# Kernel tuning notes

Hardware: AMD Instinct MI355X
Metric: run time of the kernel (lower is better)

Reference implementation:

```python
import jax, jax.numpy as jnp
import numpy as np

B, L, H, NH = 4, 2048, 1024, 8
DK = H // NH   # head_k_dim = 128
DV = H // NH   # head_v_dim = 128
CONV_K, FIR_S, FIR_L = 4, 3, 31
CMAX = 0.2
EPS = 1e-5
CHUNK = 32


def _l2norm(x):
    return x * jax.lax.rsqrt(jnp.sum(x * x, -1, keepdims=True) + 1e-6)


def _rms(x, w):
    return x * jax.lax.rsqrt(jnp.mean(x * x, -1, keepdims=True) + EPS) * w


def _causal_conv(x, w):
    # x: [b, l, d], w: [d, K] depthwise causal FIR (ShortConvolution)
    K = w.shape[1]
    l = x.shape[1]
    xp = jnp.pad(x, ((0, 0), (K - 1, 0), (0, 0)))
    return sum(xp[:, i:i + l, :] * w[:, i][None, None, :] for i in range(K))


def _fir(x, w):
    # x: [b, l, h, d], w: [h, d, K] per-head depthwise causal FIR
    K = w.shape[-1]
    l = x.shape[1]
    xp = jnp.pad(x, ((0, 0), (K - 1, 0), (0, 0), (0, 0)))
    return sum(xp[:, i:i + l] * w[:, :, i][None, None] for i in range(K))


def _delta_rule_chunkwise(q, k, v, beta, chunk=CHUNK):
    # q,k: [b,h,L,dk]; v: [b,h,L,dv]; beta: [b,h,L]; L % chunk == 0
    b, h, Ln, dk = q.shape
    dv = v.shape[-1]
    n = Ln // chunk
    q = _l2norm(q)
    k = _l2norm(k)
    v = v * beta[..., None]
    kb = k * beta[..., None]
    rs = lambda t: t.reshape(b, h, n, chunk, t.shape[-1])
    qc, kc, vc, kbc = rs(q), rs(k), rs(v), rs(kb)
    mask_incl = jnp.triu(jnp.ones((chunk, chunk), dtype=bool), 0)
    mask_strict = jnp.triu(jnp.ones((chunk, chunk), dtype=bool), 1)
    # UT / WY transform: sequential Gaussian-elimination over chunk rows
    attn = jnp.where(mask_incl, 0.0, -(kbc @ jnp.swapaxes(kc, -1, -2)))
    for i in range(1, chunk):
        row = attn[..., i, :]                                   # [b,h,n,c]
        upd = jnp.einsum('bhnj,bhnjk->bhnk', row, attn[..., :i])  # [b,h,n,i]
        attn = attn.at[..., i, :i].add(upd)
    attn = attn + jnp.eye(chunk, dtype=attn.dtype)
    u = attn @ vc    # [b,h,n,c,dv]
    w = attn @ kbc   # [b,h,n,c,dk]
    # sequential scan over chunks carrying state S [b,h,dk,dv]
    mv = lambda t: jnp.moveaxis(t, 2, 0)  # [n,b,h,c,d]
    def step(S, xs):
        q_i, k_i, u_i, w_i = xs
        attn_local = jnp.where(mask_strict, 0.0, q_i @ jnp.swapaxes(k_i, -1, -2))
        u_new = u_i - w_i @ S
        o_i = q_i @ S + attn_local @ u_new
        S = S + jnp.swapaxes(k_i, -1, -2) @ u_new
        return S, o_i
    S0 = jnp.zeros((b, h, dk, dv), dtype=q.dtype)
    S, o = jax.lax.scan(step, S0, (mv(qc), mv(kc), mv(u), mv(w)))
    o = jnp.moveaxis(o, 0, 2).reshape(b, h, Ln, dv)
    return o, S


def _forward(hidden_states, Wq, Wk, Wv, Wb, conv_q_w, conv_k_w, conv_v_w,
             fir_short_w, fir_long_w, floor_W, floor_b, fus_W1, fus_b1,
             fus_W2, fus_b2, norm_pf_w, norm_o_w, Wo):
    b, l, _ = hidden_states.shape
    hs = hidden_states
    q_lin = jax.nn.silu(_causal_conv(hs @ Wq, conv_q_w))
    k_lin = jax.nn.silu(_causal_conv(hs @ Wk, conv_k_w))
    v_lin = jax.nn.silu(_causal_conv(hs @ Wv, conv_v_w))
    q = q_lin.reshape(b, l, NH, DK)
    k = k_lin.reshape(b, l, NH, DK)
    v_direct = v_lin.reshape(b, l, NH, DV)
    beta = jax.nn.sigmoid(hs @ Wb)  # [b,l,h]
    delta_out_t, _ = _delta_rule_chunkwise(
        jnp.transpose(q, (0, 2, 1, 3)), jnp.transpose(k, (0, 2, 1, 3)),
        jnp.transpose(v_direct, (0, 2, 1, 3)), jnp.transpose(beta, (0, 2, 1)))
    delta_out = jnp.transpose(delta_out_t, (0, 2, 1, 3))  # [b,l,h,dv]
    local_short = _fir(v_direct, fir_short_w)
    local_long = _fir(v_direct, fir_long_w)
    floor = jax.nn.sigmoid(hs @ floor_W + floor_b) * CMAX  # [b,l,h]
    fus = jax.nn.gelu(hs @ fus_W1 + fus_b1, approximate=False) @ fus_W2 + fus_b2
    fus = fus.reshape(b, l, NH, 4)
    p_value = jax.nn.sigmoid(fus[..., 3]) * (1.0 - floor)  # context share >= floor
    ctx = jax.nn.softmax(fus[..., :3], axis=-1) * (1.0 - p_value)[..., None]
    o = (ctx[..., 0, None] * local_short + ctx[..., 1, None] * local_long
         + ctx[..., 2, None] * delta_out + p_value[..., None] * v_direct)
    o = _rms(o, norm_pf_w)
    o = _rms(o, norm_o_w)
    return o.reshape(b, l, NH * DV) @ Wo


def setup_inputs() -> dict:
    key = jax.random.key(0)
    ks = jax.random.split(key, 16)
    n = lambda k, shape, s=0.02: jax.random.normal(k, shape, jnp.float32) * s
    fus_b2 = jnp.zeros((NH * 4,), jnp.float32).at[3::4].set(4.0)
    return {
        'hidden_states': jax.random.normal(ks[0], (B, L, H), jnp.float32),
        'Wq': n(ks[1], (H, H)), 'Wk': n(ks[2], (H, H)), 'Wv': n(ks[3], (H, H)),
        'Wb': n(ks[4], (H, NH)),
        'conv_q_w': n(ks[5], (H, CONV_K), 0.2),
        'conv_k_w': n(ks[6], (H, CONV_K), 0.2),
        'conv_v_w': n(ks[7], (H, CONV_K), 0.2),
        'fir_short_w': n(ks[8], (NH, DV, FIR_S), 0.2),
        'fir_long_w': n(ks[9], (NH, DV, FIR_L), 0.2),
        'floor_W': n(ks[10], (H, NH)),
        'floor_b': jnp.full((NH,), float(np.log(CMAX / (1 - CMAX))), jnp.float32),
        'fus_W1': n(ks[11], (H, 2 * H)), 'fus_b1': jnp.zeros((2 * H,), jnp.float32),
        'fus_W2': n(ks[12], (2 * H, NH * 4)), 'fus_b2': fus_b2,
        'norm_pf_w': jnp.ones((DV,), jnp.float32),
        'norm_o_w': jnp.ones((DV,), jnp.float32),
        'Wo': n(ks[13], (H, H)),
    }


def reference(hidden_states, Wq, Wk, Wv, Wb, conv_q_w, conv_k_w, conv_v_w,
              fir_short_w, fir_long_w, floor_W, floor_b, fus_W1, fus_b1,
              fus_W2, fus_b2, norm_pf_w, norm_o_w, Wo):
    return _forward(hidden_states, Wq, Wk, Wv, Wb, conv_q_w, conv_k_w, conv_v_w,
                    fir_short_w, fir_long_w, floor_W, floor_b, fus_W1, fus_b1,
                    fus_W2, fus_b2, norm_pf_w, norm_o_w, Wo)
```

## Files before the change

kernel.cpp:

```cpp
#include <hip/hip_runtime.h>
#include <hip/hip_bf16.h>
#include <cstdint>
#include <cstddef>

#define DEVI static __device__ __forceinline__

typedef __attribute__((ext_vector_type(4))) float f32x4;
typedef __attribute__((ext_vector_type(8))) short s16x8;
typedef unsigned short u16;
typedef unsigned int u32;

DEVI float bf2f(u16 u){ u32 x = ((u32)u) << 16; float f; __builtin_memcpy(&f, &x, 4); return f; }
DEVI u16 f2bf(float f){ u32 x; __builtin_memcpy(&x, &f, 4); u32 r = x + 0x7fffu + ((x >> 16) & 1u); return (u16)(r >> 16); }
DEVI float sigm(float x){ return 1.0f / (1.0f + __expf(-x)); }
DEVI f32x4 mfma16(s16x8 a, s16x8 b, f32x4 c){ return __builtin_amdgcn_mfma_f32_16x16x32_bf16(a, b, c, 0, 0, 0); }
DEVI s16x8 pack8(float4 a, float4 b){
  s16x8 v;
  v[0]=(short)f2bf(a.x); v[1]=(short)f2bf(a.y); v[2]=(short)f2bf(a.z); v[3]=(short)f2bf(a.w);
  v[4]=(short)f2bf(b.x); v[5]=(short)f2bf(b.y); v[6]=(short)f2bf(b.z); v[7]=(short)f2bf(b.w);
  return v;
}
DEVI u32 pkbf(float lo, float hi){
  u32 d; asm("v_cvt_pk_bf16_f32 %0, %1, %2" : "=v"(d) : "v"(lo), "v"(hi));
  return d;
}
DEVI s16x8 ld_tr(const u16* p){
  short4 a = *(const short4*)p;
  short4 b = *(const short4*)(p + 4);
  s16x8 v; v[0]=a.x; v[1]=a.y; v[2]=a.z; v[3]=a.w; v[4]=b.x; v[5]=b.y; v[6]=b.z; v[7]=b.w;
  return v;
}

#define GLL16(gp, lp) __builtin_amdgcn_global_load_lds( \
    (const __attribute__((address_space(1))) void*)(gp), \
    (__attribute__((address_space(3))) void*)(lp), 16, 0, 0)

__global__ __launch_bounds__(256) void cvt_bf16_k(const float* __restrict__ src, u16* __restrict__ dst, int n4){
  int i = blockIdx.x * 256 + threadIdx.x;
  if (i < n4){
    float4 v = ((const float4*)src)[i];
    ushort4 o; o.x = f2bf(v.x); o.y = f2bf(v.y); o.z = f2bf(v.z); o.w = f2bf(v.w);
    ((ushort4*)dst)[i] = o;
  }
}

DEVI void transpose_tile(const float* src, u16* dst, int K, int N,
                         int n0, int k0, int t){
  __shared__ float tile[32][33];
  const int cc = t & 31, rb = t >> 5;
  #pragma unroll
  for (int it = 0; it < 4; ++it){ int rr = rb + it*8; tile[rr][cc] = src[(size_t)(k0+rr)*N + n0 + cc]; }
  __syncthreads();
  #pragma unroll
  for (int it = 0; it < 4; ++it){ int rr = rb + it*8; dst[(size_t)(n0+rr)*K + k0 + cc] = f2bf(tile[cc][rr]); }
}

__global__ __launch_bounds__(256) void prep_k(
    const float* __restrict__ Wq, const float* __restrict__ Wk, const float* __restrict__ Wv,
    const float* __restrict__ W1, const float* __restrict__ Wo,
    const float* __restrict__ W2, const float* __restrict__ Wb, const float* __restrict__ Wfl,
    u16* __restrict__ wqT, u16* __restrict__ wkT, u16* __restrict__ wvT,
    u16* __restrict__ w1T, u16* __restrict__ woT,
    u16* __restrict__ w2p, u16* __restrict__ wbp)
{
  const int blk = blockIdx.x, t = threadIdx.x;
  if (blk < 3072){
    const int which = blk >> 10, tile = blk & 1023;
    const float* src = (which == 0) ? Wq : (which == 1) ? Wk : Wv;
    u16* dst = (which == 0) ? wqT : (which == 1) ? wkT : wvT;
    transpose_tile(src, dst, 1024, 1024, (tile & 31)*32, (tile >> 5)*32, t);
  } else if (blk < 5120){
    const int tile = blk - 3072;
    transpose_tile(W1, w1T, 1024, 2048, (tile & 63)*32, (tile >> 6)*32, t);
  } else if (blk < 6144){
    const int tile = blk - 5120;
    transpose_tile(Wo, woT, 1024, 1024, (tile & 31)*32, (tile >> 5)*32, t);
  } else if (blk < 6272){
    if (t < 64){
      const int i = blk - 6144, kt = i & 63, nt = i >> 6;
      const int lane = t, g = lane >> 4, r = lane & 15;
      float v[8];
      #pragma unroll
      for (int j=0;j<8;++j) v[j] = W2[(size_t)(kt*32 + g*8 + j)*32 + nt*16 + r];
      *(s16x8*)(w2p + (((size_t)kt*2 + nt)*64 + lane)*8) =
          pack8(make_float4(v[0],v[1],v[2],v[3]), make_float4(v[4],v[5],v[6],v[7]));
    }
  } else {
    if (t < 64){
      const int kt = blk - 6272;
      const int lane = t, g = lane >> 4, r = lane & 15;
      float v[8];
      #pragma unroll
      for (int j=0;j<8;++j){
        const int k = kt*32 + g*8 + j;
        v[j] = (r < 8) ? Wb[(size_t)k*8 + r] : Wfl[(size_t)k*8 + (r-8)];
      }
      *(s16x8*)(wbp + ((size_t)kt*64 + lane)*8) =
          pack8(make_float4(v[0],v[1],v[2],v[3]), make_float4(v[4],v[5],v[6],v[7]));
    }
  }
}

template<int EPI>
__global__ __launch_bounds__(256, 2) void gemm_bt(
    const u16* __restrict__ A, const u16* __restrict__ Bt, void* __restrict__ Cout,
    const float* __restrict__ bias, int M, int N, int K)
{
  __shared__ __align__(16) u16 As[128*64];
  __shared__ __align__(16) u16 Bs[128*64];
  const int t = threadIdx.x;
  const int lane = t & 63, w = t >> 6;
  const int wr = w >> 1, wc = w & 1;
  const int g = lane >> 4, r16 = lane & 15;
  const int nwg = gridDim.x * gridDim.y;
  const int bid = blockIdx.x + blockIdx.y * gridDim.x;
  const int swz = (bid & 7) * (nwg >> 3) + (bid >> 3);
  const int m0 = (swz / gridDim.x) * 128, n0 = (swz % gridDim.x) * 128;
  f32x4 acc[4][4];
  #pragma unroll
  for (int i=0;i<4;++i){ f32x4 z = {0,0,0,0}; acc[i][0]=z; acc[i][1]=z; acc[i][2]=z; acc[i][3]=z; }
  const int NK = K / 64;
  const int slot_l = w*64 + lane;
  for (int kt = 0; kt < NK; ++kt){
    __syncthreads();
    #pragma unroll
    for (int j=0;j<4;++j){
      const int sl = j*256 + slot_l;
      const int row = sl >> 3, ch = sl & 7;
      const int chs = ch ^ (row & 7);
      GLL16(A  + (size_t)(m0+row)*K + kt*64 + chs*8, As + (size_t)(j*256 + w*64)*8);
      GLL16(Bt + (size_t)(n0+row)*K + kt*64 + chs*8, Bs + (size_t)(j*256 + w*64)*8);
    }
    __syncthreads();
    #pragma unroll
    for (int kh = 0; kh < 2; ++kh){
      s16x8 af[4], bf_[4];
      #pragma unroll
      for (int i=0;i<4;++i){
        const int arow = wr*64 + i*16 + r16;
        af[i]  = *(const s16x8*)(As + (size_t)arow*64 + (((4*kh+g) ^ (arow&7)))*8);
        const int brow = wc*64 + i*16 + r16;
        bf_[i] = *(const s16x8*)(Bs + (size_t)brow*64 + (((4*kh+g) ^ (brow&7)))*8);
      }
      #pragma unroll
      for (int mi=0;mi<4;++mi)
        #pragma unroll
        for (int ni=0;ni<4;++ni)
          acc[mi][ni] = mfma16(af[mi], bf_[ni], acc[mi][ni]);
    }
  }
  #pragma unroll
  for (int mi=0;mi<4;++mi)
    #pragma unroll
    for (int ni=0;ni<4;++ni){
      const int col = n0 + wc*64 + ni*16 + r16;
      #pragma unroll
      for (int i=0;i<4;++i){
        const int row = m0 + wr*64 + mi*16 + g*4 + i;
        float v = acc[mi][ni][i];
        if (EPI == 0){
          ((u16*)Cout)[(size_t)row*N + col] = f2bf(v);
        } else if (EPI == 1){
          float x = v + bias[col];
          x = 0.5f * x * (1.0f + erff(x * 0.70710678118f));
          ((u16*)Cout)[(size_t)row*N + col] = f2bf(x);
        } else if (EPI == 2){
          ((float*)Cout)[(size_t)row*N + col] = v;
        } else {
          ((u16*)Cout)[(size_t)(col >> 10)*8388608 + (size_t)row*1024 + (col & 1023)] = f2bf(v);
        }
      }
    }
}

__global__ __launch_bounds__(64) void beta_floor_k(
    const u16* __restrict__ hsb, const u16* __restrict__ wbp, const float* __restrict__ flb,
    float* __restrict__ beta, float* __restrict__ flo)
{
  const int m0 = blockIdx.x * 16;
  const int lane = threadIdx.x, g = lane >> 4, r = lane & 15;
  f32x4 acc0 = {0,0,0,0}, acc1 = {0,0,0,0};
  #pragma unroll 4
  for (int kt = 0; kt < 32; kt += 2){
    s16x8 a0 = *(const s16x8*)(hsb + (size_t)(m0+r)*1024 + kt*32 + g*8);
    s16x8 b0 = *(const s16x8*)(wbp + ((size_t)kt*64 + lane)*8);
    s16x8 a1 = *(const s16x8*)(hsb + (size_t)(m0+r)*1024 + (kt+1)*32 + g*8);
    s16x8 b1 = *(const s16x8*)(wbp + ((size_t)(kt+1)*64 + lane)*8);
    acc0 = mfma16(a0, b0, acc0);
    acc1 = mfma16(a1, b1, acc1);
  }
  const float fb = (r >= 8) ? flb[r-8] : 0.f;
  #pragma unroll
  for (int i=0;i<4;++i){
    const int row = m0 + g*4 + i;
    const float v = acc0[i] + acc1[i];
    if (r < 8) beta[(size_t)row*8 + r] = sigm(v);
    else       flo [(size_t)row*8 + (r-8)] = 0.2f * sigm(v + fb);
  }
}

__global__ __launch_bounds__(256) void conv_silu_k(
    const u16* __restrict__ qraw, const u16* __restrict__ kraw, const u16* __restrict__ vraw,
    const float* __restrict__ cwq, const float* __restrict__ cwk, const float* __restrict__ cwv,
    u16* __restrict__ vdir, u16* __restrict__ qn, u16* __restrict__ kn)
{
  const int blk = blockIdx.x;
  const int b = blk >> 7, lt = blk & 127;
  const int l0 = lt * 16;
  const int t = threadIdx.x, c0 = t * 4;
  float wq[16], wk[16], wv[16];
  #pragma unroll
  for (int cc=0; cc<4; ++cc){
    float4 a = *(const float4*)(cwq + (size_t)(c0+cc)*4);
    wq[cc*4+0]=a.x; wq[cc*4+1]=a.y; wq[cc*4+2]=a.z; wq[cc*4+3]=a.w;
    float4 bq = *(const float4*)(cwk + (size_t)(c0+cc)*4);
    wk[cc*4+0]=bq.x; wk[cc*4+1]=bq.y; wk[cc*4+2]=bq.z; wk[cc*4+3]=bq.w;
    float4 c = *(const float4*)(cwv + (size_t)(c0+cc)*4);
    wv[cc*4+0]=c.x; wv[cc*4+1]=c.y; wv[cc*4+2]=c.z; wv[cc*4+3]=c.w;
  }
  float hq[3][4], hk[3][4], hv[3][4];
  #pragma unroll
  for (int i=0;i<3;++i){
    const int ls = l0 - 3 + i;
    if (ls >= 0){
      const size_t base = ((size_t)(b << 11) + ls)*1024 + c0;
      union{ ushort4 v; u16 s[4]; } xq, xk, xv;
      xq.v = *(const ushort4*)(qraw + base);
      xk.v = *(const ushort4*)(kraw + base);
      xv.v = *(const ushort4*)(vraw + base);
      #pragma unroll
      for (int cc=0;cc<4;++cc){ hq[i][cc]=bf2f(xq.s[cc]); hk[i][cc]=bf2f(xk.s[cc]); hv[i][cc]=bf2f(xv.s[cc]); }
    } else {
      #pragma unroll
      for (int cc=0;cc<4;++cc){ hq[i][cc]=0.f; hk[i][cc]=0.f; hv[i][cc]=0.f; }
    }
  }
  float cq[4], ck4[4], cv4[4], nq[4], nk[4], nv[4];
  {
    const size_t base = ((size_t)(b << 11) + l0)*1024 + c0;
    union{ ushort4 v; u16 s[4]; } xq, xk, xv;
    xq.v = *(const ushort4*)(qraw + base);
    xk.v = *(const ushort4*)(kraw + base);
    xv.v = *(const ushort4*)(vraw + base);
    #pragma unroll
    for (int cc=0;cc<4;++cc){ cq[cc]=bf2f(xq.s[cc]); ck4[cc]=bf2f(xk.s[cc]); cv4[cc]=bf2f(xv.s[cc]); }
  }
  const int head = c0 >> 7, d0 = c0 & 127;
  for (int rr = 0; rr < 16; ++rr){
    const int l = l0 + rr;
    if (rr < 15){
      const size_t base = ((size_t)(b << 11) + l + 1)*1024 + c0;
      union{ ushort4 v; u16 s[4]; } xq, xk, xv;
      xq.v = *(const ushort4*)(qraw + base);
      xk.v = *(const ushort4*)(kraw + base);
      xv.v = *(const ushort4*)(vraw + base);
      #pragma unroll
      for (int cc=0;cc<4;++cc){ nq[cc]=bf2f(xq.s[cc]); nk[cc]=bf2f(xk.s[cc]); nv[cc]=bf2f(xv.s[cc]); }
    }
    float qa[4], ka[4], va[4];
    #pragma unroll
    for (int cc=0; cc<4; ++cc){
      qa[cc] = hq[0][cc]*wq[cc*4+0] + hq[1][cc]*wq[cc*4+1] + hq[2][cc]*wq[cc*4+2] + cq[cc]*wq[cc*4+3];
      ka[cc] = hk[0][cc]*wk[cc*4+0] + hk[1][cc]*wk[cc*4+1] + hk[2][cc]*wk[cc*4+2] + ck4[cc]*wk[cc*4+3];
      va[cc] = hv[0][cc]*wv[cc*4+0] + hv[1][cc]*wv[cc*4+1] + hv[2][cc]*wv[cc*4+2] + cv4[cc]*wv[cc*4+3];
    }
    #pragma unroll
    for (int cc=0; cc<4; ++cc){
      qa[cc] = qa[cc]*sigm(qa[cc]); ka[cc] = ka[cc]*sigm(ka[cc]); va[cc] = va[cc]*sigm(va[cc]);
    }
    const int grow = (b << 11) + l;
    ushort4 ov; ov.x=f2bf(va[0]); ov.y=f2bf(va[1]); ov.z=f2bf(va[2]); ov.w=f2bf(va[3]);
    *(ushort4*)(vdir + (size_t)grow*1024 + c0) = ov;
    float ssq = 0.f, ssk = 0.f;
    #pragma unroll
    for (int cc=0; cc<4; ++cc){ ssq += qa[cc]*qa[cc]; ssk += ka[cc]*ka[cc]; }
    #pragma unroll
    for (int m=1; m<32; m<<=1){ ssq += __shfl_xor(ssq, m, 64); ssk += __shfl_xor(ssk, m, 64); }
    const float rq = rsqrtf(ssq + 1e-6f), rk = rsqrtf(ssk + 1e-6f);
    const size_t ob = (((size_t)(b*8 + head))*2048 + l)*128 + d0;
    ushort4 oq, ok;
    oq.x=f2bf(qa[0]*rq); oq.y=f2bf(qa[1]*rq); oq.z=f2bf(qa[2]*rq); oq.w=f2bf(qa[3]*rq);
    ok.x=f2bf(ka[0]*rk); ok.y=f2bf(ka[1]*rk); ok.z=f2bf(ka[2]*rk); ok.w=f2bf(ka[3]*rk);
    *(ushort4*)(qn + ob) = oq;
    *(ushort4*)(kn + ob) = ok;
    #pragma unroll
    for (int cc=0; cc<4; ++cc){
      hq[0][cc]=hq[1][cc]; hq[1][cc]=hq[2][cc]; hq[2][cc]=cq[cc];  cq[cc]=nq[cc];
      hk[0][cc]=hk[1][cc]; hk[1][cc]=hk[2][cc]; hk[2][cc]=ck4[cc]; ck4[cc]=nk[cc];
      hv[0][cc]=hv[1][cc]; hv[1][cc]=hv[2][cc]; hv[2][cc]=cv4[cc]; cv4[cc]=nv[cc];
    }
  }
}

__global__ __launch_bounds__(64) void fus2_k(
    const u16* __restrict__ A, const u16* __restrict__ w2p, const float* __restrict__ b2,
    float* __restrict__ out)
{
  const int m0 = blockIdx.x * 16;
  const int lane = threadIdx.x, g = lane >> 4, r = lane & 15;
  f32x4 acc[2][2];
  #pragma unroll
  for (int nt=0;nt<2;++nt){ f32x4 z = {0,0,0,0}; acc[nt][0]=z; acc[nt][1]=z; }
  #pragma unroll 4
  for (int kt = 0; kt < 64; ++kt){
    s16x8 af = *(const s16x8*)(A + (size_t)(m0+r)*2048 + kt*32 + g*8);
    s16x8 b0 = *(const s16x8*)(w2p + (((size_t)kt*2 + 0)*64 + lane)*8);
    s16x8 b1 = *(const s16x8*)(w2p + (((size_t)kt*2 + 1)*64 + lane)*8);
    acc[0][kt&1] = mfma16(af, b0, acc[0][kt&1]);
    acc[1][kt&1] = mfma16(af, b1, acc[1][kt&1]);
  }
  #pragma unroll
  for (int nt=0;nt<2;++nt){
    const float bb = b2[nt*16 + r];
    #pragma unroll
    for (int i=0;i<4;++i)
      out[(size_t)(m0 + g*4 + i)*32 + nt*16 + r] = acc[nt][0][i] + acc[nt][1][i] + bb;
  }
}

__global__ __launch_bounds__(256, 2) void ut_k(
    const u16* __restrict__ qn, const u16* __restrict__ kn,
    const u16* __restrict__ vdir, const float* __restrict__ beta,
    u16* __restrict__ alocp, u16* __restrict__ updk,
    u16* __restrict__ wpk, u16* __restrict__ knpk, u16* __restrict__ qpk)
{
  __shared__ __align__(16) char smem[39680];
  u16*  k_s = (u16*)smem;
  float* Tm = (float*)smem;
  float* Gm = (float*)(smem + 8192);
  float* al = (float*)(smem + 12416);
  float* wl = (float*)(smem + 8192);
  u16*  knT = (u16*)(smem + 17024);
  u16*  vbT = (u16*)(smem + 28288);
  float* bet = (float*)(smem + 39552);

  const int blk = blockIdx.x;
  const int ic = blk & 63, bh = blk >> 6;
  const int b = bh >> 3, h = bh & 7;
  const int l0 = ic * 32;
  const int t = threadIdx.x;
  const int lane = t & 63, w = t >> 6;
  const int g = lane >> 4, r = lane & 15;
  const int mt = w >> 1, nt_g = w & 1;

  const size_t gqk = ((size_t)bh*2048 + l0)*128;

  {
    const int row = t >> 3, sseg = t & 7;
    #pragma unroll
    for (int ss=0; ss<2; ++ss){
      const int s = sseg + ss*8;
      int4 kv = *(const int4*)(kn + gqk + (size_t)row*128 + s*8);
      *(int4*)((char*)k_s + row*256 + ((s ^ (row&7))*16)) = kv;
    }
  }
  {
    const int rp = t & 15, cs = t >> 4;
    const int r0 = 2*rp, r1 = 2*rp + 1;
    union { s16x8 v; u16 u[8]; } k0, k1, v0, v1;
    k0.v = *(const s16x8*)(kn + gqk + (size_t)r0*128 + cs*8);
    k1.v = *(const s16x8*)(kn + gqk + (size_t)r1*128 + cs*8);
    v0.v = *(const s16x8*)(vdir + ((size_t)b*2048 + l0 + r0)*1024 + h*128 + cs*8);
    v1.v = *(const s16x8*)(vdir + ((size_t)b*2048 + l0 + r1)*1024 + h*128 + cs*8);
    const float be0 = beta[((size_t)b*2048 + l0 + r0)*8 + h];
    const float be1 = beta[((size_t)b*2048 + l0 + r1)*8 + h];
    if (t < 32) bet[t] = beta[((size_t)b*2048 + l0 + t)*8 + h];
    #pragma unroll
    for (int i=0;i<8;++i){
      const int d = cs*8 + i;
      *(u32*)(knT + (size_t)d*44 + r0) = (u32)k0.u[i] | ((u32)k1.u[i] << 16);
      u32 lo = f2bf(bf2f(v0.u[i]) * be0);
      u32 hi = f2bf(bf2f(v1.u[i]) * be1);
      *(u32*)(vbT + (size_t)d*44 + r0) = lo | (hi << 16);
    }
  }
  __syncthreads();

  {
    f32x4 gacc = {0,0,0,0}, aacc = {0,0,0,0};
    #pragma unroll
    for (int kt=0; kt<4; ++kt){
      s16x8 afk = *(const s16x8*)(kn + gqk + (size_t)(mt*16+r)*128 + kt*32 + g*8);
      s16x8 afq = *(const s16x8*)(qn + gqk + (size_t)(mt*16+r)*128 + kt*32 + g*8);
      if (nt_g == 0)
        *(s16x8*)(qpk + ((((size_t)blk*2 + mt)*4 + kt)*64 + lane)*8) = afq;
      const int brow = nt_g*16 + r;
      s16x8 bfrag = *(const s16x8*)((const char*)k_s + brow*256 + (((kt*4+g) ^ (brow&7))*16));
      gacc = mfma16(afk, bfrag, gacc);
      aacc = mfma16(afq, bfrag, aacc);
    }
    #pragma unroll
    for (int i=0;i<4;++i){
      const int rr = mt*16 + g*4 + i, cc = nt_g*16 + r;
      Gm[rr*33 + cc] = gacc[i];
      al[rr*36 + cc] = (cc <= rr) ? aacc[i] : 0.f;
    }
  }
  __syncthreads();

  if (w == 0){
    const int kk = lane & 15, grp = (lane >> 4) & 1, b0 = grp*16;
    float tc[16];
    #pragma unroll
    for (int j=0;j<16;++j)
      tc[j] = (j > kk) ? (-bet[b0+j] * Gm[(b0+j)*33 + b0+kk]) : 0.f;
    #pragma unroll
    for (int i=1;i<16;++i){
      float upd = 0.f;
      #pragma unroll
      for (int j=0;j<i;++j) upd += __shfl(tc[i], (lane & 48) + j, 64) * tc[j];
      if (kk < i) tc[i] += upd;
    }
    if (lane < 32){
      #pragma unroll
      for (int j=0;j<16;++j) Tm[(b0+j)*36 + b0+kk] = tc[j] + ((j == kk) ? 1.f : 0.f);
      if (grp == 1){
        #pragma unroll
        for (int j=0;j<16;++j) Tm[j*36 + 16 + kk] = 0.f;
      }
    }
  } else if (w == 1){
    #pragma unroll
    for (int m2=0; m2<2; ++m2){
      float4 z0 = *(const float4*)(al + (m2*16+r)*36 + g*8);
      float4 z1 = *(const float4*)(al + (m2*16+r)*36 + g*8 + 4);
      *(s16x8*)(alocp + (((size_t)blk*2 + m2)*64 + lane)*8) = pack8(z0, z1);
    }
  } else {
    #pragma unroll
    for (int q2=0; q2<4; ++q2){
      const int mtd = (w-2)*4 + q2;
      s16x8 vv = ld_tr(knT + (size_t)(mtd*16+r)*44 + g*8);
      *(s16x8*)(knpk + (((size_t)blk*8 + mtd)*64 + lane)*8) = vv;
    }
  }
  __syncthreads();

  {
    const int kP = t >> 4, cP = t & 15;
    float p = 0.f;
    #pragma unroll
    for (int m=0;m<16;++m) p += Gm[(16+kP)*33 + m] * Tm[m*36 + cP];
    al[kP*36 + cP] = -bet[16+kP] * p;
  }
  __syncthreads();

  {
    const int rT = t >> 4, cT = t & 15;
    float s = 0.f;
    #pragma unroll
    for (int k=0;k<16;++k) s += Tm[(16+rT)*36 + 16 + k] * al[k*36 + cT];
    Tm[(16+rT)*36 + cT] = s;
  }
  __syncthreads();

  {
    float bb[8];
    #pragma unroll
    for (int i=0;i<8;++i) bb[i] = bet[g*8+i];
    s16x8 tA[2];
    #pragma unroll
    for (int m2=0; m2<2; ++m2){
      float4 x0 = *(const float4*)(Tm + (m2*16+r)*36 + g*8);
      float4 x1 = *(const float4*)(Tm + (m2*16+r)*36 + g*8 + 4);
      tA[m2] = pack8(x0, x1);
    }
    #pragma unroll
    for (int rr2=0; rr2<2; ++rr2){
      const int nt = rr2*4 + w;
      s16x8 bu   = ld_tr(vbT + (size_t)(nt*16+r)*44 + g*8);
      s16x8 braw = ld_tr(knT + (size_t)(nt*16+r)*44 + g*8);
      s16x8 bw;
      #pragma unroll
      for (int i=0;i<8;++i) bw[i] = (short)f2bf(bf2f((u16)braw[i]) * bb[i]);
      f32x4 zz = {0,0,0,0};
      f32x4 du0 = mfma16(tA[0], bu, zz);
      f32x4 du1 = mfma16(tA[1], bu, zz);
      f32x4 dw0 = mfma16(tA[0], bw, zz);
      f32x4 dw1 = mfma16(tA[1], bw, zz);
      *(s16x8*)(updk + (((size_t)blk*8 + nt)*64 + lane)*8) =
          pack8(make_float4(du0[0],du0[1],du0[2],du0[3]),
                make_float4(du1[0],du1[1],du1[2],du1[3]));
      #pragma unroll
      for (int i=0;i<4;++i){
        wl[(      g*4 + i)*68 + (nt&3)*16 + r] = -dw0[i];
        wl[(16 +  g*4 + i)*68 + (nt&3)*16 + r] = -dw1[i];
      }
      __syncthreads();
      {
        const int mtp = w >> 1, ktp = rr2*2 + (w & 1);
        float4 y0 = *(const float4*)(wl + (mtp*16+r)*68 + (ktp&1)*32 + g*8);
        float4 y1 = *(const float4*)(wl + (mtp*16+r)*68 + (ktp&1)*32 + g*8 + 4);
        *(s16x8*)(wpk + ((((size_t)blk*2 + mtp)*4 + ktp)*64 + lane)*8) = pack8(y0, y1);
      }
      __syncthreads();
    }
  }
}

struct SBuf {
  s16x8 uraw;
  s16x8 wf[8];
  s16x8 qf[8];
  s16x8 a0, a1;
  s16x8 kf[8];
};

DEVI void scan_load(SBuf& b, const u16* up, const u16* wp, const u16* qp,
                    const u16* ap, const u16* kp){
  b.uraw = *(const s16x8*)(up);
  #pragma unroll
  for (int j=0;j<8;++j) b.wf[j] = *(const s16x8*)(wp + j*512);
  #pragma unroll
  for (int j=0;j<8;++j) b.qf[j] = *(const s16x8*)(qp + j*512);
  b.a0 = *(const s16x8*)(ap);
  b.a1 = *(const s16x8*)(ap + 512);
  #pragma unroll
  for (int j=0;j<8;++j) b.kf[j] = *(const s16x8*)(kp + j*512);
}

DEVI void scan_step(const SBuf& b, f32x4* Sf, u16* dptr,
                    int srcA, int srcB, bool hi, int r, int g){
  u32 pk0[8], pk1[8];
  #pragma unroll
  for (int m=0;m<8;++m){
    pk0[m] = pkbf(Sf[m][0], Sf[m][1]);
    pk1[m] = pkbf(Sf[m][2], Sf[m][3]);
  }
  s16x8 sf[4];
  #pragma unroll
  for (int kt=0;kt<4;++kt){
    u32 eA0 = __shfl(pk0[kt*2],   srcA, 64), oA0 = __shfl(pk0[kt*2+1], srcA, 64);
    u32 eA1 = __shfl(pk1[kt*2],   srcA, 64), oA1 = __shfl(pk1[kt*2+1], srcA, 64);
    u32 eB0 = __shfl(pk0[kt*2],   srcB, 64), oB0 = __shfl(pk0[kt*2+1], srcB, 64);
    u32 eB1 = __shfl(pk1[kt*2],   srcB, 64), oB1 = __shfl(pk1[kt*2+1], srcB, 64);
    union { u32 w[4]; s16x8 v; } uw;
    uw.w[0] = hi ? oA0 : eA0;
    uw.w[1] = hi ? oA1 : eA1;
    uw.w[2] = hi ? oB0 : eB0;
    uw.w[3] = hi ? oB1 : eB1;
    sf[kt] = uw.v;
  }
  f32x4 unA, unB, unA2 = {0,0,0,0}, unB2 = {0,0,0,0};
  #pragma unroll
  for (int i=0;i<4;++i){ unA[i] = bf2f((u16)b.uraw[i]); unB[i] = bf2f((u16)b.uraw[4+i]); }
  unA  = mfma16(b.wf[0], sf[0], unA);
  unA2 = mfma16(b.wf[2], sf[2], unA2);
  unB  = mfma16(b.wf[4], sf[0], unB);
  unB2 = mfma16(b.wf[6], sf[2], unB2);
  unA  = mfma16(b.wf[1], sf[1], unA);
  unA2 = mfma16(b.wf[3], sf[3], unA2);
  unB  = mfma16(b.wf[5], sf[1], unB);
  unB2 = mfma16(b.wf[7], sf[3], unB2);
  f32x4 o0 = {0,0,0,0}, o1 = {0,0,0,0};
  #pragma unroll
  for (int kt=0;kt<4;++kt){
    o0 = mfma16(b.qf[kt],   sf[kt], o0);
    o1 = mfma16(b.qf[4+kt], sf[kt], o1);
  }
  unA = unA + unA2;
  unB = unB + unB2;
  u32 a0p0 = pkbf(unA[0], unA[1]), a0p1 = pkbf(unA[2], unA[3]);
  u32 a1p0 = pkbf(unB[0], unB[1]), a1p1 = pkbf(unB[2], unB[3]);
  u32 w00 = __shfl(a0p0, srcA, 64), w10 = __shfl(a1p0, srcA, 64);
  u32 w01 = __shfl(a0p1, srcA, 64), w11 = __shfl(a1p1, srcA, 64);
  u32 w02 = __shfl(a0p0, srcB, 64), w12 = __shfl(a1p0, srcB, 64);
  u32 w03 = __shfl(a0p1, srcB, 64), w13 = __shfl(a1p1, srcB, 64);
  union { u32 w[4]; s16x8 v; } uu;
  uu.w[0] = hi ? w10 : w00;
  uu.w[1] = hi ? w11 : w01;
  uu.w[2] = hi ? w12 : w02;
  uu.w[3] = hi ? w13 : w03;
  const s16x8 uf = uu.v;
  o0 = mfma16(b.a0, uf, o0);
  o1 = mfma16(b.a1, uf, o1);
  #pragma unroll
  for (int i=0;i<4;++i){
    dptr[(size_t)(g*4+i)*128]    = f2bf(o0[i]);
    dptr[(size_t)(16+g*4+i)*128] = f2bf(o1[i]);
  }
  #pragma unroll
  for (int m=0;m<8;++m) Sf[m] = mfma16(b.kf[m], uf, Sf[m]);
}

__global__ __launch_bounds__(64, 1) void scan_k(
    const u16* __restrict__ qpk, const u16* __restrict__ wpk,
    const u16* __restrict__ updk, const u16* __restrict__ alocp,
    const u16* __restrict__ knpk, u16* __restrict__ delta)
{
  const int blk = blockIdx.x;
  const int sl = blk >> 5, bh = blk & 31;
  const int lane = threadIdx.x;
  const int g = lane >> 4, r = lane & 15;
  const int srcA = (g & 1)*32 + r;
  const int srcB = srcA + 16;
  const bool hi = (g >= 2);
  f32x4 Sf[8];
  #pragma unroll
  for (int m=0;m<8;++m){ f32x4 z = {0,0,0,0}; Sf[m] = z; }

  const u16* upB = updk + ((size_t)bh*64*8 + sl)*512 + (size_t)lane*8;
  const u16* wpB = wpk  + (size_t)bh*64*4096 + (size_t)lane*8;
  const u16* qpB = qpk  + (size_t)bh*64*4096 + (size_t)lane*8;
  const u16* apB = alocp + (size_t)bh*64*1024 + (size_t)lane*8;
  const u16* kpB = knpk + (size_t)bh*64*4096 + (size_t)lane*8;
  u16*       dB  = delta + (size_t)bh*2048*128 + sl*16 + r;

  #define LD(buf, n) scan_load(buf, upB + (size_t)(n)*4096, wpB + (size_t)(n)*4096, \
                               qpB + (size_t)(n)*4096, apB + (size_t)(n)*1024, \
                               kpB + (size_t)(n)*4096)
  #define ST(buf, n) scan_step(buf, Sf, dB + (size_t)(n)*4096, srcA, srcB, hi, r, g)

  SBuf A, B, C;
  LD(A, 0); LD(B, 1);
  for (int ic = 0; ic < 63; ic += 3){
    LD(C, ic+2);
    ST(A, ic);
    if (ic + 3 < 64) LD(A, ic+3);
    ST(B, ic+1);
    if (ic + 4 < 64) LD(B, ic+4);
    ST(C, ic+2);
  }
  ST(A, 63);
  #undef LD
  #undef ST
}

__global__ __launch_bounds__(256) void fuse_k(
    const u16* __restrict__ vdir, const u16* __restrict__ delta,
    const float* __restrict__ fusv, const float* __restrict__ flo,
    const float* __restrict__ fsw, const float* __restrict__ flw,
    const float* __restrict__ wpf, const float* __restrict__ wno,
    u16* __restrict__ ofin)
{
  __shared__ float fl_t[31][128];
  const int blk = blockIdx.x;
  const int lt = blk & 31, h = (blk >> 5) & 7, b = blk >> 8;
  const int t = threadIdx.x;
  const int w = t >> 6, lane = t & 63;
  const int d0 = lane * 2;
  const int l0 = lt*64 + w*16;
  for (int j = t; j < 3968; j += 256){
    const int d = j / 31, i = j - d*31;
    fl_t[i][d] = flw[(size_t)h*3968 + j];
  }
  __syncthreads();
  float wlo[46], whi[46];
  #pragma unroll
  for (int j = 0; j < 46; ++j){
    const int ls = l0 - 30 + j;
    u32 x = 0;
    if (ls >= 0) x = *(const u32*)(vdir + ((size_t)b*2048 + ls)*1024 + h*128 + d0);
    wlo[j] = bf2f((u16)(x & 0xffffu));
    whi[j] = bf2f((u16)(x >> 16));
  }
  float lg0[16], lg1[16];
  #pragma unroll
  for (int rr = 0; rr < 16; ++rr){ lg0[rr] = 0.f; lg1[rr] = 0.f; }
  #pragma unroll
  for (int i = 0; i < 31; ++i){
    const float2 wv = *(const float2*)&fl_t[i][d0];
    #pragma unroll
    for (int rr = 0; rr < 16; ++rr){
      lg0[rr] += wlo[rr + i] * wv.x;
      lg1[rr] += whi[rr + i] * wv.y;
    }
  }
  const float wp0 = wpf[d0], wp1 = wpf[d0+1];
  const float wn0 = wno[d0], wn1 = wno[d0+1];
  float fs0[3], fs1[3];
  #pragma unroll
  for (int i=0;i<3;++i){
    fs0[i] = fsw[((size_t)h*128 + d0)*3 + i];
    fs1[i] = fsw[((size_t)h*128 + d0 + 1)*3 + i];
  }
  #pragma unroll
  for (int rr = 0; rr < 16; ++rr){
    const int l = l0 + rr;
    const float* fr = fusv + ((size_t)b*2048 + l)*32 + h*4;
    const float f0=fr[0], f1=fr[1], f2=fr[2], f3=fr[3];
    const float flv = flo[((size_t)b*2048 + l)*8 + h];
    const float p = sigm(f3) * (1.f - flv);
    const float mx = fmaxf(f0, fmaxf(f1, f2));
    const float e0 = __expf(f0-mx), e1 = __expf(f1-mx), e2 = __expf(f2-mx);
    const float inv = (1.f - p) / (e0 + e1 + e2);
    const float c0 = e0*inv, c1 = e1*inv, c2 = e2*inv;
    const float sh0 = wlo[rr+28]*fs0[0] + wlo[rr+29]*fs0[1] + wlo[rr+30]*fs0[2];
    const float sh1 = whi[rr+28]*fs1[0] + whi[rr+29]*fs1[1] + whi[rr+30]*fs1[2];
    const u32 dl2 = *(const u32*)(delta + (((size_t)(b*8 + h))*2048 + l)*128 + d0);
    const float dlx = bf2f((u16)(dl2 & 0xffffu)), dly = bf2f((u16)(dl2 >> 16));
    float o0 = c0*sh0 + c1*lg0[rr] + c2*dlx + p*wlo[rr+30];
    float o1 = c0*sh1 + c1*lg1[rr] + c2*dly + p*whi[rr+30];
    const float b0 = o0*wp0, b1 = o1*wp1;
    float ss = o0*o0 + o1*o1;
    float tt = b0*b0 + b1*b1;
    #pragma unroll
    for (int m=1; m<64; m<<=1){
      ss += __shfl_xor(ss, m, 64);
      tt += __shfl_xor(tt, m, 64);
    }
    const float r1 = rsqrtf(ss * (1.f/128.f) + 1e-5f);
    const float r2 = rsqrtf(r1*r1*tt * (1.f/128.f) + 1e-5f);
    const u32 h0 = f2bf(o0*r1*wp0*r2*wn0), h1 = f2bf(o1*r1*wp1*r2*wn1);
    *(u32*)(ofin + ((size_t)b*2048 + l)*1024 + h*128 + d0) = h0 | (h1 << 16);
  }
}

constexpr size_t OFF_HSB  = 0;
constexpr size_t OFF_WQT  = 16777216;
constexpr size_t OFF_WKT  = 18874368;
constexpr size_t OFF_WVT  = 20971520;
constexpr size_t OFF_W1T  = 23068672;
constexpr size_t OFF_WOT  = 27262976;
constexpr size_t OFF_QRAW = 29360128;
constexpr size_t OFF_KRAW = 46137344;
constexpr size_t OFF_VRAW = 62914560;
constexpr size_t OFF_FUSV = 79691776;
constexpr size_t OFF_BETA = 80740352;
constexpr size_t OFF_FLO  = 81002496;
constexpr size_t OFF_VDIR = 81264640;
constexpr size_t OFF_W2P  = 98041856;
constexpr size_t OFF_WBP  = 98172928;
constexpr size_t OFF_QN   = 114819072;
constexpr size_t OFF_KN   = 131596288;
constexpr size_t OFF_ALOC = 148373504;
constexpr size_t OFF_UPDK = 152567808;
constexpr size_t OFF_KNPK = 186122240;

extern "C" void kernel_launch(void* const* d_in, const int* in_sizes, int n_in,
                              void* d_out, int out_size, void* d_ws, size_t ws_size,
                              hipStream_t stream)
{
  const float* hs   = (const float*)d_in[0];
  const float* Wq   = (const float*)d_in[1];
  const float* Wk   = (const float*)d_in[2];
  const float* Wv   = (const float*)d_in[3];
  const float* Wb   = (const float*)d_in[4];
  const float* cq   = (const float*)d_in[5];
  const float* ck   = (const float*)d_in[6];
  const float* cv   = (const float*)d_in[7];
  const float* firs = (const float*)d_in[8];
  const float* firl = (const float*)d_in[9];
  const float* flW  = (const float*)d_in[10];
  const float* flb  = (const float*)d_in[11];
  const float* W1   = (const float*)d_in[12];
  const float* b1   = (const float*)d_in[13];
  const float* W2   = (const float*)d_in[14];
  const float* b2   = (const float*)d_in[15];
  const float* npf  = (const float*)d_in[16];
  const float* now  = (const float*)d_in[17];
  const float* Wo   = (const float*)d_in[18];

  char* ws = (char*)d_ws;
  u16*   hsb   = (u16*)(ws + OFF_HSB);
  u16*   wqT   = (u16*)(ws + OFF_WQT);
  u16*   wkT   = (u16*)(ws + OFF_WKT);
  u16*   wvT   = (u16*)(ws + OFF_WVT);
  u16*   w1T   = (u16*)(ws + OFF_W1T);
  u16*   woT   = (u16*)(ws + OFF_WOT);
  u16*   qraw  = (u16*)(ws + OFF_QRAW);
  u16*   kraw  = (u16*)(ws + OFF_KRAW);
  u16*   vraw  = (u16*)(ws + OFF_VRAW);
  u16*   fus1g = (u16*)(ws + OFF_QRAW);
  float* fusv  = (float*)(ws + OFF_FUSV);
  float* beta  = (float*)(ws + OFF_BETA);
  float* flo   = (float*)(ws + OFF_FLO);
  u16*   vdir  = (u16*)(ws + OFF_VDIR);
  u16*   w2p   = (u16*)(ws + OFF_W2P);
  u16*   wbp   = (u16*)(ws + OFF_WBP);
  u16*   qn    = (u16*)(ws + OFF_QN);
  u16*   kn    = (u16*)(ws + OFF_KN);
  u16*   alocp = (u16*)(ws + OFF_ALOC);
  u16*   updk  = (u16*)(ws + OFF_UPDK);
  u16*   wpk   = (u16*)(ws + OFF_VRAW);
  u16*   knpk  = (u16*)(ws + OFF_KNPK);
  u16*   qpk   = (u16*)(ws + OFF_HSB);
  u16*   delta = (u16*)(ws + OFF_QRAW);
  u16*   ofin  = (u16*)(ws + OFF_UPDK);

  cvt_bf16_k<<<8192, 256, 0, stream>>>(hs, hsb, 2097152);
  prep_k<<<6304, 256, 0, stream>>>(Wq, Wk, Wv, W1, Wo, W2, Wb, flW,
                                   wqT, wkT, wvT, w1T, woT, w2p, wbp);
  beta_floor_k<<<512, 64, 0, stream>>>(hsb, wbp, flb, beta, flo);
  gemm_bt<3><<<dim3(24,64), 256, 0, stream>>>(hsb, wqT, qraw, nullptr, 8192, 3072, 1024);
  conv_silu_k<<<512, 256, 0, stream>>>(qraw, kraw, vraw, cq, ck, cv, vdir, qn, kn);
  gemm_bt<1><<<dim3(16,64), 256, 0, stream>>>(hsb, w1T, fus1g, b1, 8192, 2048, 1024);
  fus2_k<<<512, 64, 0, stream>>>(fus1g, w2p, b2, fusv);
  ut_k<<<2048, 256, 0, stream>>>(qn, kn, vdir, beta, alocp, updk, wpk, knpk, qpk);
  scan_k<<<256, 64, 0, stream>>>(qpk, wpk, updk, alocp, knpk, delta);
  fuse_k<<<1024, 256, 0, stream>>>(vdir, delta, fusv, flo, firs, firl, npf, now, ofin);
  gemm_bt<2><<<dim3(8,64), 256, 0, stream>>>(ofin, woT, d_out, nullptr, 8192, 1024, 1024);
}
```

Baseline: 331.3 us.

## Fold beta/floor projection into QKV GEMM and merge bf16 cast into prep

New measurement: 333.8 us. Within noise of the previous version (+0.8%).

```diff
diff --git a/kernel.cpp b/kernel.cpp
--- a/kernel.cpp
+++ b/kernel.cpp
@@ -35,15 +35,6 @@
     (const __attribute__((address_space(1))) void*)(gp), \
     (__attribute__((address_space(3))) void*)(lp), 16, 0, 0)
 
-__global__ __launch_bounds__(256) void cvt_bf16_k(const float* __restrict__ src, u16* __restrict__ dst, int n4){
-  int i = blockIdx.x * 256 + threadIdx.x;
-  if (i < n4){
-    float4 v = ((const float4*)src)[i];
-    ushort4 o; o.x = f2bf(v.x); o.y = f2bf(v.y); o.z = f2bf(v.z); o.w = f2bf(v.w);
-    ((ushort4*)dst)[i] = o;
-  }
-}
-
 DEVI void transpose_tile(const float* src, u16* dst, int K, int N,
                          int n0, int k0, int t){
   __shared__ float tile[32][33];
@@ -59,9 +50,10 @@
     const float* __restrict__ Wq, const float* __restrict__ Wk, const float* __restrict__ Wv,
     const float* __restrict__ W1, const float* __restrict__ Wo,
     const float* __restrict__ W2, const float* __restrict__ Wb, const float* __restrict__ Wfl,
+    const float* __restrict__ hs,
     u16* __restrict__ wqT, u16* __restrict__ wkT, u16* __restrict__ wvT,
     u16* __restrict__ w1T, u16* __restrict__ woT,
-    u16* __restrict__ w2p, u16* __restrict__ wbp)
+    u16* __restrict__ w2p, u16* __restrict__ wbfT, u16* __restrict__ hsb)
 {
   const int blk = blockIdx.x, t = threadIdx.x;
   if (blk < 3072){
@@ -85,26 +77,28 @@
       *(s16x8*)(w2p + (((size_t)kt*2 + nt)*64 + lane)*8) =
           pack8(make_float4(v[0],v[1],v[2],v[3]), make_float4(v[4],v[5],v[6],v[7]));
     }
+  } else if (blk < 6288){
+    const int i = blk - 6272;
+    for (int e = t; e < 8*1024; e += 256){
+      const int row = i*8 + (e >> 10), k = e & 1023;
+      float v = 0.f;
+      if (row < 8) v = Wb[(size_t)k*8 + row];
+      else if (row < 16) v = Wfl[(size_t)k*8 + (row-8)];
+      wbfT[(size_t)row*1024 + k] = f2bf(v);
+    }
   } else {
-    if (t < 64){
-      const int kt = blk - 6272;
-      const int lane = t, g = lane >> 4, r = lane & 15;
-      float v[8];
-      #pragma unroll
-      for (int j=0;j<8;++j){
-        const int k = kt*32 + g*8 + j;
-        v[j] = (r < 8) ? Wb[(size_t)k*8 + r] : Wfl[(size_t)k*8 + (r-8)];
-      }
-      *(s16x8*)(wbp + ((size_t)kt*64 + lane)*8) =
-          pack8(make_float4(v[0],v[1],v[2],v[3]), make_float4(v[4],v[5],v[6],v[7]));
-    }
+    const int i = (blk - 6288)*256 + t;
+    float4 v = ((const float4*)hs)[i];
+    ushort4 o; o.x = f2bf(v.x); o.y = f2bf(v.y); o.z = f2bf(v.z); o.w = f2bf(v.w);
+    ((ushort4*)hsb)[i] = o;
   }
 }
 
 template<int EPI>
 __global__ __launch_bounds__(256, 2) void gemm_bt(
-    const u16* __restrict__ A, const u16* __restrict__ Bt, void* __restrict__ Cout,
-    const float* __restrict__ bias, int M, int N, int K)
+    const u16* __restrict__ A, const u16* __restrict__ Bt, const u16* __restrict__ Bt2,
+    void* __restrict__ Cout, const float* __restrict__ bias,
+    float* __restrict__ betap, float* __restrict__ flop, int M, int N, int K)
 {
   __shared__ __align__(16) u16 As[128*64];
   __shared__ __align__(16) u16 Bs[128*64];
@@ -116,6 +110,7 @@
   const int bid = blockIdx.x + blockIdx.y * gridDim.x;
   const int swz = (bid & 7) * (nwg >> 3) + (bid >> 3);
   const int m0 = (swz / gridDim.x) * 128, n0 = (swz % gridDim.x) * 128;
+  const bool btile = (EPI == 3) && (n0 >= 3072);
   f32x4 acc[4][4];
   #pragma unroll
   for (int i=0;i<4;++i){ f32x4 z = {0,0,0,0}; acc[i][0]=z; acc[i][1]=z; acc[i][2]=z; acc[i][3]=z; }
@@ -128,8 +123,10 @@
       const int sl = j*256 + slot_l;
       const int row = sl >> 3, ch = sl & 7;
       const int chs = ch ^ (row & 7);
-      GLL16(A  + (size_t)(m0+row)*K + kt*64 + chs*8, As + (size_t)(j*256 + w*64)*8);
-      GLL16(Bt + (size_t)(n0+row)*K + kt*64 + chs*8, Bs + (size_t)(j*256 + w*64)*8);
+      GLL16(A + (size_t)(m0+row)*K + kt*64 + chs*8, As + (size_t)(j*256 + w*64)*8);
+      const u16* bp = btile ? (Bt2 + (size_t)row*1024 + kt*64 + chs*8)
+                            : (Bt + (size_t)(n0+row)*K + kt*64 + chs*8);
+      GLL16(bp, Bs + (size_t)(j*256 + w*64)*8);
     }
     __syncthreads();
     #pragma unroll
@@ -158,45 +155,23 @@
       for (int i=0;i<4;++i){
         const int row = m0 + wr*64 + mi*16 + g*4 + i;
         float v = acc[mi][ni][i];
-        if (EPI == 0){
-          ((u16*)Cout)[(size_t)row*N + col] = f2bf(v);
-        } else if (EPI == 1){
+        if (EPI == 1){
           float x = v + bias[col];
           x = 0.5f * x * (1.0f + erff(x * 0.70710678118f));
           ((u16*)Cout)[(size_t)row*N + col] = f2bf(x);
         } else if (EPI == 2){
           ((float*)Cout)[(size_t)row*N + col] = v;
         } else {
-          ((u16*)Cout)[(size_t)(col >> 10)*8388608 + (size_t)row*1024 + (col & 1023)] = f2bf(v);
+          if (col < 3072){
+            ((u16*)Cout)[(size_t)(col >> 10)*8388608 + (size_t)row*1024 + (col & 1023)] = f2bf(v);
+          } else {
+            const int j = col - 3072;
+            if (j < 8)       betap[(size_t)row*8 + j] = sigm(v);
+            else if (j < 16) flop[(size_t)row*8 + (j-8)] = 0.2f * sigm(v + bias[j-8]);
+          }
         }
       }
     }
-}
-
-__global__ __launch_bounds__(64) void beta_floor_k(
-    const u16* __restrict__ hsb, const u16* __restrict__ wbp, const float* __restrict__ flb,
-    float* __restrict__ beta, float* __restrict__ flo)
-{
-  const int m0 = blockIdx.x * 16;
-  const int lane = threadIdx.x, g = lane >> 4, r = lane & 15;
-  f32x4 acc0 = {0,0,0,0}, acc1 = {0,0,0,0};
-  #pragma unroll 4
-  for (int kt = 0; kt < 32; kt += 2){
-    s16x8 a0 = *(const s16x8*)(hsb + (size_t)(m0+r)*1024 + kt*32 + g*8);
-    s16x8 b0 = *(const s16x8*)(wbp + ((size_t)kt*64 + lane)*8);
-    s16x8 a1 = *(const s16x8*)(hsb + (size_t)(m0+r)*1024 + (kt+1)*32 + g*8);
-    s16x8 b1 = *(const s16x8*)(wbp + ((size_t)(kt+1)*64 + lane)*8);
-    acc0 = mfma16(a0, b0, acc0);
-    acc1 = mfma16(a1, b1, acc1);
-  }
-  const float fb = (r >= 8) ? flb[r-8] : 0.f;
-  #pragma unroll
-  for (int i=0;i<4;++i){
-    const int row = m0 + g*4 + i;
-    const float v = acc0[i] + acc1[i];
-    if (r < 8) beta[(size_t)row*8 + r] = sigm(v);
-    else       flo [(size_t)row*8 + (r-8)] = 0.2f * sigm(v + fb);
-  }
 }
 
 __global__ __launch_bounds__(256) void conv_silu_k(
@@ -720,7 +695,7 @@
 constexpr size_t OFF_FLO  = 81002496;
 constexpr size_t OFF_VDIR = 81264640;
 constexpr size_t OFF_W2P  = 98041856;
-constexpr size_t OFF_WBP  = 98172928;
+constexpr size_t OFF_WBFT = 98205696;
 constexpr size_t OFF_QN   = 114819072;
 constexpr size_t OFF_KN   = 131596288;
 constexpr size_t OFF_ALOC = 148373504;
@@ -767,7 +742,7 @@
   float* flo   = (float*)(ws + OFF_FLO);
   u16*   vdir  = (u16*)(ws + OFF_VDIR);
   u16*   w2p   = (u16*)(ws + OFF_W2P);
-  u16*   wbp   = (u16*)(ws + OFF_WBP);
+  u16*   wbfT  = (u16*)(ws + OFF_WBFT);
   u16*   qn    = (u16*)(ws + OFF_QN);
   u16*   kn    = (u16*)(ws + OFF_KN);
   u16*   alocp = (u16*)(ws + OFF_ALOC);
@@ -778,16 +753,17 @@
   u16*   delta = (u16*)(ws + OFF_QRAW);
   u16*   ofin  = (u16*)(ws + OFF_UPDK);
 
-  cvt_bf16_k<<<8192, 256, 0, stream>>>(hs, hsb, 2097152);
-  prep_k<<<6304, 256, 0, stream>>>(Wq, Wk, Wv, W1, Wo, W2, Wb, flW,
-                                   wqT, wkT, wvT, w1T, woT, w2p, wbp);
-  beta_floor_k<<<512, 64, 0, stream>>>(hsb, wbp, flb, beta, flo);
-  gemm_bt<3><<<dim3(24,64), 256, 0, stream>>>(hsb, wqT, qraw, nullptr, 8192, 3072, 1024);
+  prep_k<<<14480, 256, 0, stream>>>(Wq, Wk, Wv, W1, Wo, W2, Wb, flW, hs,
+                                    wqT, wkT, wvT, w1T, woT, w2p, wbfT, hsb);
+  gemm_bt<3><<<dim3(25,64), 256, 0, stream>>>(hsb, wqT, wbfT, qraw, flb,
+                                              beta, flo, 8192, 3200, 1024);
   conv_silu_k<<<512, 256, 0, stream>>>(qraw, kraw, vraw, cq, ck, cv, vdir, qn, kn);
-  gemm_bt<1><<<dim3(16,64), 256, 0, stream>>>(hsb, w1T, fus1g, b1, 8192, 2048, 1024);
+  gemm_bt<1><<<dim3(16,64), 256, 0, stream>>>(hsb, w1T, nullptr, fus1g, b1,
+                                              nullptr, nullptr, 8192, 2048, 1024);
   fus2_k<<<512, 64, 0, stream>>>(fus1g, w2p, b2, fusv);
   ut_k<<<2048, 256, 0, stream>>>(qn, kn, vdir, beta, alocp, updk, wpk, knpk, qpk);
   scan_k<<<256, 64, 0, stream>>>(qpk, wpk, updk, alocp, knpk, delta);
   fuse_k<<<1024, 256, 0, stream>>>(vdir, delta, fusv, flo, firs, firl, npf, now, ofin);
-  gemm_bt<2><<<dim3(8,64), 256, 0, stream>>>(ofin, woT, d_out, nullptr, 8192, 1024, 1024);
-}
+  gemm_bt<2><<<dim3(8,64), 256, 0, stream>>>(ofin, woT, nullptr, d_out, nullptr,
+                                             nullptr, nullptr, 8192, 1024, 1024);
+}
```
